# Performance work log

Measured on AMD Instinct MI355X. Metric: run time of the kernel, lower is better.

The kernel has to match this reference:

```python
import jax, jax.numpy as jnp
import numpy as np

B_, G_, H_ = 16, 4096, 128
D_INNER, D_STATE, NHEADS, HEADDIM, CHUNK, D_CONV = 256, 16, 4, 64, 64, 4
LATENT = 64
D_IN_PROJ = 2 * D_INNER + 2 * D_STATE + NHEADS  # 548
CONV_DIM = D_INNER + 2 * D_STATE                # 288
NLAYERS = 4  # [fwd0, fwd1, bwd0, bwd1]
EPS = 1e-5


def _segsum(x):
    # x: (..., T) -> (..., T, T) stable segment sums, -inf above diagonal
    T = x.shape[-1]
    xe = jnp.broadcast_to(x[..., None], x.shape + (T,))
    lo = jnp.tril(jnp.ones((T, T), bool), -1)
    s = jnp.cumsum(jnp.where(lo, xe, 0.0), axis=-2)
    keep = jnp.tril(jnp.ones((T, T), bool), 0)
    return jnp.where(keep, s, -jnp.inf)


def _ssd(x, A, B, C):
    # x: (b, L, h, p), A: (b, L, h), B/C: (b, L, n)  (single shared head for B/C)
    b, L, h, p = x.shape
    c = L // CHUNK
    x = x.reshape(b, c, CHUNK, h, p)
    A = A.reshape(b, c, CHUNK, h).transpose(0, 3, 1, 2)  # b h c l
    B = B.reshape(b, c, CHUNK, -1)                       # b c l n
    C = C.reshape(b, c, CHUNK, -1)
    A_cs = jnp.cumsum(A, axis=-1)
    Lmat = jnp.exp(_segsum(A))                           # b h c l s
    Y_diag = jnp.einsum('bcln,bcsn,bhcls,bcshp->bclhp', C, B, Lmat, x)
    decay_states = jnp.exp(A_cs[:, :, :, -1:] - A_cs)
    states = jnp.einsum('bcln,bhcl,bclhp->bchpn', B, decay_states, x)
    states = jnp.concatenate([jnp.zeros_like(states[:, :1]), states], axis=1)
    decay_chunk = jnp.exp(_segsum(jnp.pad(A_cs[:, :, :, -1], ((0, 0), (0, 0), (1, 0)))))
    new_states = jnp.einsum('bhzc,bchpn->bzhpn', decay_chunk, states)
    states = new_states[:, :-1]
    sdo = jnp.exp(A_cs)
    Y_off = jnp.einsum('bcln,bchpn,bhcl->bclhp', C, states, sdo)
    return (Y_diag + Y_off).reshape(b, L, h, p)


def _mamba2(u, Wi, cw, cb, dtb, Alog, Dp, nw, Wo):
    b, L, _ = u.shape
    zxbcdt = u @ Wi.T                                   # (b, L, 548)
    z = zxbcdt[..., :D_INNER]
    xBC = zxbcdt[..., D_INNER:D_INNER + CONV_DIM]
    dt = jax.nn.softplus(zxbcdt[..., D_INNER + CONV_DIM:] + dtb)  # (b, L, h)
    # depthwise causal conv1d, padding=d_conv-1, keep first L outputs
    xt = xBC.transpose(0, 2, 1)
    y = jax.lax.conv_general_dilated(xt, cw[:, None, :], (1,), [(D_CONV - 1, D_CONV - 1)],
                                     dimension_numbers=('NCH', 'OIH', 'NCH'),
                                     feature_group_count=CONV_DIM)
    xBC = jax.nn.silu((y[:, :, :L] + cb[None, :, None]).transpose(0, 2, 1))
    x = xBC[..., :D_INNER].reshape(b, L, NHEADS, HEADDIM)
    Bm = xBC[..., D_INNER:D_INNER + D_STATE]
    Cm = xBC[..., D_INNER + D_STATE:]
    A = -jnp.exp(Alog)                                  # (h,)
    yssd = _ssd(x * dt[..., None], A * dt, Bm, Cm)
    yssd = yssd + x * Dp[:, None]
    yf = yssd.reshape(b, L, D_INNER)
    yf = yf * jax.nn.silu(z)                            # gated RMSNorm
    yf = yf * jax.lax.rsqrt(jnp.mean(yf * yf, -1, keepdims=True) + EPS) * nw
    return yf @ Wo.T


def _forward(expression, noise, expr_w, expr_b, in_proj_w, conv_w, conv_b, dt_bias,
             A_log, D_par, norm_w, out_proj_w, fusion_w, fusion_b, lm_w, lm_b,
             lv_w, lv_b, gate_w, gate_b, outp_w, outp_b, reg_gate):
    x = expression[..., None] * expr_w[:, 0] + expr_b   # Linear(1, H) -> (b, G, H)
    fwd = x
    for i in (0, 1):
        fwd = _mamba2(fwd, in_proj_w[i], conv_w[i], conv_b[i], dt_bias[i],
                      A_log[i], D_par[i], norm_w[i], out_proj_w[i])
    bwd = x[:, ::-1]
    for i in (2, 3):
        bwd = _mamba2(bwd, in_proj_w[i], conv_w[i], conv_b[i], dt_bias[i],
                      A_log[i], D_par[i], norm_w[i], out_proj_w[i])
    bwd = bwd[:, ::-1]
    fused = jax.nn.gelu(jnp.concatenate([fwd, bwd], -1) @ fusion_w.T + fusion_b,
                        approximate=False)
    lm = fused @ lm_w.T + lm_b
    lv = fused @ lv_w.T + lv_b
    sample = lm + noise * jnp.exp(0.5 * lv)             # reparameterize
    gate = jax.nn.sigmoid(sample @ gate_w.T + gate_b)
    h = fused * gate
    pred = (h @ outp_w.T + outp_b)[..., 0] * jax.nn.sigmoid(reg_gate)
    return pred, lm, lv, sample


def setup_inputs() -> dict:
    key = jax.random.key(0)
    ks = jax.random.split(key, 24)
    def w(k, shape, s=0.02):
        return jax.random.normal(k, shape, jnp.float32) * s
    return dict(
        expression=jax.random.uniform(ks[0], (B_, G_), jnp.float32),
        noise=jax.random.normal(ks[1], (B_, G_, LATENT), jnp.float32),
        expr_w=w(ks[2], (H_, 1), 0.2), expr_b=w(ks[3], (H_,)),
        in_proj_w=w(ks[4], (NLAYERS, D_IN_PROJ, H_)),
        conv_w=w(ks[5], (NLAYERS, CONV_DIM, D_CONV), 0.1),
        conv_b=w(ks[6], (NLAYERS, CONV_DIM)),
        dt_bias=jax.random.uniform(ks[7], (NLAYERS, NHEADS), jnp.float32, -4.0, 1.0),
        A_log=jnp.full((NLAYERS, NHEADS), -jnp.log(2.0), jnp.float32),
        D_par=jnp.ones((NLAYERS, NHEADS), jnp.float32),
        norm_w=jnp.ones((NLAYERS, D_INNER), jnp.float32),
        out_proj_w=w(ks[8], (NLAYERS, H_, D_INNER)),
        fusion_w=w(ks[9], (H_, 2 * H_)), fusion_b=w(ks[10], (H_,)),
        lm_w=w(ks[11], (LATENT, H_)), lm_b=w(ks[12], (LATENT,)),
        lv_w=w(ks[13], (LATENT, H_)), lv_b=w(ks[14], (LATENT,)),
        gate_w=w(ks[15], (H_, LATENT)), gate_b=w(ks[16], (H_,)),
        outp_w=w(ks[17], (1, H_)), outp_b=w(ks[18], (1,)),
        reg_gate=w(ks[19], (G_,), 0.01),
    )


def reference(expression, noise, expr_w, expr_b, in_proj_w, conv_w, conv_b, dt_bias,
              A_log, D_par, norm_w, out_proj_w, fusion_w, fusion_b, lm_w, lm_b,
              lv_w, lv_b, gate_w, gate_b, outp_w, outp_b, reg_gate):
    return _forward(expression, noise, expr_w, expr_b, in_proj_w, conv_w, conv_b,
                    dt_bias, A_log, D_par, norm_w, out_proj_w, fusion_w, fusion_b,
                    lm_w, lm_b, lv_w, lv_b, gate_w, gate_b, outp_w, outp_b, reg_gate)
```

## Files before the change

kernel.cpp:

```cpp
#include <hip/hip_runtime.h>
#include <math.h>

#define HMOD 128
#define DIN 256
#define NHEADS 4
#define HD 64
#define DSTATE 16
#define NCH 64
#define CONVD 288
#define DPROJ 548
#define LAT 64
#define LSEQ 4096

typedef __attribute__((ext_vector_type(8))) short bf16x8;
typedef __attribute__((ext_vector_type(4))) float f32x4;
typedef __attribute__((ext_vector_type(8))) unsigned short u16x8;

__device__ __forceinline__ float sigm(float x){ return 1.0f/(1.0f+__expf(-x)); }
__device__ __forceinline__ float siluf(float x){ return x/(1.0f+__expf(-x)); }
__device__ __forceinline__ float softplusf(float x){ return (x>20.0f)? x : log1pf(expf(x)); }
__device__ __forceinline__ float geluf(float x){ return 0.5f*x*(1.0f+erff(x*0.70710678118654752440f)); }
__device__ __forceinline__ unsigned short f2bf(float x){
  unsigned int u = __float_as_uint(x);
  return (unsigned short)((u + 0x7FFFu + ((u>>16)&1u)) >> 16);
}
__device__ __forceinline__ float bf2f(unsigned short h){
  return __uint_as_float(((unsigned int)h)<<16);
}

__global__ __launch_bounds__(256) void cvt_kernel(const float* __restrict__ in,
  unsigned short* __restrict__ out, int n)
{
  int i = blockIdx.x*256 + threadIdx.x;
  if (i < n) out[i] = f2bf(in[i]);
}
__global__ __launch_bounds__(256) void cvt_nw_kernel(const float* __restrict__ in,
  const float* __restrict__ nw, unsigned short* __restrict__ out, int n)
{
  int i = blockIdx.x*256 + threadIdx.x;
  if (i < n){
    int k = i & 255;
    int li = i >> 15;
    out[i] = f2bf(in[i]*nw[li*256 + k]);
  }
}
__global__ __launch_bounds__(256) void cvt_cw_kernel(const float* __restrict__ in,
  float* __restrict__ out)
{
  int i = blockIdx.x*256 + threadIdx.x;
  if (i < 4608){
    int li = i/1152, r = i - li*1152;
    int ch = r>>2, k = r&3;
    out[li*1152 + k*CONVD + ch] = in[i];
  }
}

__global__ __launch_bounds__(256) void embed_kernel(const float* __restrict__ expr,
    const float* __restrict__ ew, const float* __restrict__ eb,
    unsigned short* __restrict__ actA, unsigned short* __restrict__ actB)
{
  int gid = blockIdx.x*256 + threadIdx.x;
  int m = gid >> 7, hh = gid & 127;
  int bl = m >> 12, g = m & 4095;
  unsigned short v = f2bf(expr[m]*ew[hh] + eb[hh]);
  actA[gid] = v;
  actB[(size_t)(((bl<<12) | (4095-g))<<7) + hh] = v;
}

template<int KDIM, int NT, int EPI>
__global__ __launch_bounds__(256) void gemm3(
    const unsigned short* __restrict__ A,
    const unsigned short* __restrict__ A2,
    const unsigned short* __restrict__ Wb,
    const float* __restrict__ bias,
    const float* __restrict__ bias2,
    const float* __restrict__ ssqp,
    unsigned short* __restrict__ ob1,
    unsigned short* __restrict__ ob2,
    float* __restrict__ of1,
    float* __restrict__ of2,
    const float* __restrict__ nzp,
    float* __restrict__ of3,
    int N, int ldc)
{
  __shared__ unsigned short Ws[64*(KDIM+8)];
  __shared__ unsigned short Cb[(EPI==5) ? 8 : 128*72];
  const int tid = threadIdx.x;
  const int m0 = blockIdx.x<<7;
  const int wid = tid>>6, lane = tid&63;
  const int la = lane&15, kq = lane>>4;
  const int mw = m0 + wid*32;

  bf16x8 af[KDIM/32][2];
  #pragma unroll
  for (int ki=0; ki<KDIM/32; ki++){
    int k = ki*32 + kq*8;
    #pragma unroll
    for (int mf=0; mf<2; mf++){
      int row = mw + mf*16 + la;
      const unsigned short* src;
      if (EPI==2){
        if (k < 128) src = A + (size_t)row*128 + k;
        else { int bl2=row>>12, t=row&4095; src = A2 + (size_t)(((bl2<<12)|(4095-t)))*128 + (k-128); }
      } else {
        src = A + (size_t)row*KDIM + k;
      }
      af[ki][mf] = *(const bf16x8*)src;
    }
  }
  float scv[2][4];
  if (EPI==4){
    #pragma unroll
    for (int mf=0; mf<2; mf++)
      #pragma unroll
      for (int r=0; r<4; r++){
        int m = mw + mf*16 + kq*4 + r;
        float s = ssqp[m*4]+ssqp[m*4+1]+ssqp[m*4+2]+ssqp[m*4+3];
        scv[mf][r] = rsqrtf(s*(1.0f/256.0f) + 1e-5f);
      }
  }
  float vlm[2][4][4];

  const int KD8 = KDIM/8;
  for (int nt=0; nt<NT; nt++){
    int n0 = (blockIdx.y*NT + nt)<<6;
    for (int ci = tid; ci < 64*KD8; ci += 256){
      int row = ci/KD8, kc = (ci - row*KD8)*8;
      int n = n0 + row;
      bf16x8 v = {0,0,0,0,0,0,0,0};
      if (n < N) v = *(const bf16x8*)&Wb[(size_t)n*KDIM + kc];
      *(bf16x8*)&Ws[row*(KDIM+8) + kc] = v;
    }
    __syncthreads();
    f32x4 acc[2][4] = {};
    #pragma unroll
    for (int ki=0; ki<KDIM/32; ki++){
      #pragma unroll
      for (int nf=0; nf<4; nf++){
        bf16x8 bfr = *(const bf16x8*)&Ws[(nf*16 + la)*(KDIM+8) + ki*32 + kq*8];
        #pragma unroll
        for (int mf=0; mf<2; mf++)
          acc[mf][nf] = __builtin_amdgcn_mfma_f32_16x16x32_bf16(af[ki][mf], bfr, acc[mf][nf], 0,0,0);
      }
    }
    #pragma unroll
    for (int mf=0; mf<2; mf++){
      #pragma unroll
      for (int nf=0; nf<4; nf++){
        #pragma unroll
        for (int r=0; r<4; r++){
          int m = mw + mf*16 + kq*4 + r;
          int row = wid*32 + mf*16 + kq*4 + r;
          int n = n0 + nf*16 + la;
          int col = nf*16 + la;
          float v = acc[mf][nf][r];
          if (EPI==1){
            if (n >= DIN+CONVD && n < DPROJ)
              of1[(size_t)m*NHEADS + (n-DIN-CONVD)] = softplusf(v + bias[n-DIN-CONVD]);
            else
              Cb[row*72 + col] = f2bf(v);
          } else if (EPI==2){
            Cb[row*72 + col] = f2bf(geluf(v + bias[n]));
          } else if (EPI==4){
            Cb[row*72 + col] = f2bf(v*scv[mf][r]);
          } else if (EPI==5){
            if (nt == 0){
              float lm = v + bias[col];
              vlm[mf][nf][r] = lm;
              of1[(size_t)m*64 + col] = lm;
            } else {
              float lv = v + bias2[col];
              of2[(size_t)m*64 + col] = lv;
              float nzv = nzp[(size_t)m*64 + col];
              of3[(size_t)m*64 + col] = fmaf(nzv, expf(0.5f*lv), vlm[mf][nf][r]);
            }
          }
        }
      }
    }
    if (EPI!=5){
      __syncthreads();
      #pragma unroll
      for (int j=0; j<4; j++){
        int row = (tid>>3) + j*32;
        int col0 = (tid&7)*8;
        int m = m0 + row;
        int nch = n0 + col0;
        u16x8 val = *(const u16x8*)&Cb[row*72 + col0];
        if (EPI==1){
          if (nch < DIN)            *(u16x8*)&ob1[(size_t)m*DIN + nch] = val;
          else if (nch < DIN+CONVD) *(u16x8*)&ob2[(size_t)m*CONVD + (nch-DIN)] = val;
        } else {
          *(u16x8*)&ob1[(size_t)m*ldc + nch] = val;
        }
      }
    }
    __syncthreads();
  }
}

__global__ __launch_bounds__(256) void conv_kernel(const unsigned short* __restrict__ xraw,
  const float* __restrict__ cwT, const float* __restrict__ cb,
  unsigned short* __restrict__ xconv)
{
  int gid = blockIdx.x*256 + threadIdx.x;
  int m = gid / 36, v = gid - (gid/36)*36;
  int ch0 = v*8;
  int t = m & 4095;
  float acc[8];
  float4 b0 = *(const float4*)&cb[ch0];
  float4 b1 = *(const float4*)&cb[ch0+4];
  acc[0]=b0.x; acc[1]=b0.y; acc[2]=b0.z; acc[3]=b0.w;
  acc[4]=b1.x; acc[5]=b1.y; acc[6]=b1.z; acc[7]=b1.w;
  #pragma unroll
  for (int k=0;k<4;k++){
    int tt = t - 3 + k;
    if (tt >= 0){
      u16x8 xv = *(const u16x8*)&xraw[(size_t)(m-3+k)*CONVD + ch0];
      float4 w0 = *(const float4*)&cwT[k*CONVD + ch0];
      float4 w1 = *(const float4*)&cwT[k*CONVD + ch0 + 4];
      float w[8] = {w0.x,w0.y,w0.z,w0.w,w1.x,w1.y,w1.z,w1.w};
      #pragma unroll
      for (int j=0;j<8;j++) acc[j] = fmaf(w[j], bf2f(xv[j]), acc[j]);
    }
  }
  u16x8 o;
  #pragma unroll
  for (int j=0;j<8;j++) o[j] = f2bf(siluf(acc[j]));
  *(u16x8*)&xconv[(size_t)m*CONVD + ch0] = o;
}

__global__ __launch_bounds__(256) void ssd_front(
  const unsigned short* __restrict__ xconv, const float* __restrict__ dtsp,
  const float* __restrict__ Alog,
  float* __restrict__ states_g, float* __restrict__ acs_g, float* __restrict__ atot_g)
{
  __shared__ __align__(16) unsigned short Xt[64*88];
  __shared__ __align__(16) unsigned short Raw[64*72];
  __shared__ __align__(16) unsigned short Braw[64*24];
  __shared__ __align__(16) unsigned short Bwt[16*88];
  __shared__ float acs_s[64], dts_s[64];
  const int bx = blockIdx.x;
  const int h = bx & 3, c = (bx>>2)&63, bl = bx>>8;
  const int tid = threadIdx.x;
  const int tokbase = (bl<<12) + (c<<6);

  if (tid < 64) {
    float dt = dtsp[(size_t)(tokbase+tid)*NHEADS + h];
    dts_s[tid] = dt;
    float xsc = -__expf(Alog[h]) * dt;
    #pragma unroll
    for (int off=1; off<64; off<<=1){ float v = __shfl_up(xsc, off); if (tid >= off) xsc += v; }
    acs_s[tid] = xsc;
    acs_g[(size_t)bx*64 + tid] = xsc;
  }
  #pragma unroll
  for (int i=0;i<2;i++){
    int idx = tid + (i<<8);
    int l = idx>>3, g = idx&7;
    *(u16x8*)&Raw[l*72 + g*8] = *(const u16x8*)&xconv[(size_t)(tokbase+l)*CONVD + h*64 + g*8];
  }
  if (tid < 128){
    int l = tid>>1, half = tid&1;
    *(u16x8*)&Braw[l*24 + half*8] = *(const u16x8*)&xconv[(size_t)(tokbase+l)*CONVD + 256 + half*8];
  }
  __syncthreads();
  const float atotv = acs_s[63];
  if (tid==0) atot_g[bx] = atotv;
  #pragma unroll
  for (int i=0;i<2;i++){
    int u = tid + (i<<8);
    int ch = u & 63, l0 = (u>>6)*8;
    u16x8 o;
    #pragma unroll
    for (int j=0;j<8;j++) o[j] = Raw[(l0+j)*72 + ch];
    *(u16x8*)&Xt[ch*88 + l0] = o;
  }
  if (tid < 128){
    int ch = tid & 15, l0 = (tid>>4)*8;
    u16x8 o;
    #pragma unroll
    for (int j=0;j<8;j++){
      int l = l0+j;
      o[j] = f2bf(bf2f(Braw[l*24 + ch]) * __expf(atotv - acs_s[l]) * dts_s[l]);
    }
    *(u16x8*)&Bwt[ch*88 + l0] = o;
  }
  __syncthreads();
  const int wid = tid>>6, lane = tid&63;
  const int la = lane&15, kq = lane>>4;
  f32x4 acc = {0.f,0.f,0.f,0.f};
  #pragma unroll
  for (int kt=0; kt<2; kt++){
    bf16x8 a = *(const bf16x8*)&Xt[(wid*16+la)*88 + kt*32+kq*8];
    bf16x8 b = *(const bf16x8*)&Bwt[la*88 + kt*32+kq*8];
    acc = __builtin_amdgcn_mfma_f32_16x16x32_bf16(a, b, acc, 0,0,0);
  }
  size_t base = (size_t)bx<<10;
  #pragma unroll
  for (int r=0;r<4;r++){
    int p = wid*16 + kq*4 + r;
    states_g[base + (size_t)p*16 + la] = acc[r];
  }
}

__global__ __launch_bounds__(256) void scan_kernel(float* __restrict__ states,
  const float* __restrict__ atot)
{
  int gid = blockIdx.x*256 + threadIdx.x;
  int inner = gid & 1023;
  int h = (gid>>10)&3;
  int bl = gid>>12;
  size_t base = (size_t)bl*262144 + h*1024 + inner;
  int abase = bl*256 + h;
  float v[64];
  #pragma unroll
  for (int c2=0;c2<64;c2++) v[c2] = states[base + (size_t)c2*4096];
  float S = 0.0f;
  #pragma unroll
  for (int c2=0;c2<64;c2++){
    states[base + (size_t)c2*4096] = S;
    S = __expf(atot[abase + c2*4])*S + v[c2];
  }
}

__global__ __launch_bounds__(256) void ssd_back(
  const unsigned short* __restrict__ xconv, const unsigned short* __restrict__ zb,
  const float* __restrict__ dtsp, const float* __restrict__ acs_g,
  const float* __restrict__ states, const float* __restrict__ Dp,
  unsigned short* __restrict__ yf, float* __restrict__ ssqp)
{
  __shared__ __align__(16) unsigned short U[2*64*72];
  __shared__ __align__(16) unsigned short CBS[3*64*40];
  __shared__ float acs_s[64], dts_s[64];
  unsigned short* Xt = U;
  unsigned short* Sb = U + 64*72;
  unsigned short* Cp = CBS;
  unsigned short* Bp = CBS + 64*40;
  unsigned short* Sp = CBS + 2*64*40;
  float* Yl = (float*)U;
  const int bx = blockIdx.x;
  const int h = bx & 3, c = (bx>>2)&63, bl = bx>>8;
  const int tid = threadIdx.x;
  const int tokbase = (bl<<12) + (c<<6);

  if (tid < 64) {
    dts_s[tid] = dtsp[(size_t)(tokbase+tid)*NHEADS + h];
    acs_s[tid] = acs_g[(size_t)bx*64 + tid];
  }
  for (int i = tid; i < 1024; i += 256){
    int l = i>>4, k = 16 + (i&15);
    Cp[l*40+k] = 0; Bp[l*40+k] = 0; Sp[l*40+k] = 0;
  }
  #pragma unroll
  for (int i=0;i<2;i++){
    int idx = tid + (i<<8);
    int l = idx>>3, g = idx&7;
    *(u16x8*)&Sb[l*72 + g*8] = *(const u16x8*)&xconv[(size_t)(tokbase+l)*CONVD + h*64 + g*8];
  }
  {
    int l = tid>>2, part = tid&3;
    u16x8 vv = *(const u16x8*)&xconv[(size_t)(tokbase+l)*CONVD + 256 + part*8];
    if (part < 2) *(u16x8*)&Bp[l*40 + part*8] = vv;
    else          *(u16x8*)&Cp[l*40 + (part-2)*8] = vv;
  }
  #pragma unroll
  for (int i=0;i<4;i++){
    int e = tid + (i<<8);
    int p = e>>4, n = e&15;
    Sp[p*40+n] = f2bf(states[((size_t)bx<<10) + e]);
  }
  __syncthreads();
  #pragma unroll
  for (int i=0;i<2;i++){
    int u = tid + (i<<8);
    int ch = u & 63, l0 = (u>>6)*8;
    u16x8 o;
    #pragma unroll
    for (int j=0;j<8;j++) o[j] = Sb[(l0+j)*72 + ch];
    *(u16x8*)&Xt[ch*72 + l0] = o;
  }
  __syncthreads();

  const int wid = tid>>6, lane = tid&63;
  const int la = lane&15, kq = lane>>4;
  const int L0 = wid*16;
  const f32x4 zero4 = {0.f,0.f,0.f,0.f};
  const float Dh = Dp[h];

  {
    bf16x8 a = *(const bf16x8*)&Cp[(L0+la)*40 + kq*8];
    f32x4 cbacc[4];
    #pragma unroll
    for (int nf=0; nf<4; nf++){
      bf16x8 b = *(const bf16x8*)&Bp[(nf*16+la)*40 + kq*8];
      cbacc[nf] = __builtin_amdgcn_mfma_f32_16x16x32_bf16(a, b, zero4, 0,0,0);
    }
    #pragma unroll
    for (int nf=0; nf<4; nf++){
      #pragma unroll
      for (int r=0; r<4; r++){
        int l = L0 + kq*4 + r, s = nf*16 + la;
        float v = 0.f;
        if (s <= l) v = __expf(acs_s[l]-acs_s[s])*dts_s[s]*cbacc[nf][r];
        if (s == l) v += Dh;
        Sb[l*72 + s] = f2bf(v);
      }
    }
  }
  f32x4 ya[4];
  {
    bf16x8 a = *(const bf16x8*)&Cp[(L0+la)*40 + kq*8];
    #pragma unroll
    for (int nf=0; nf<4; nf++){
      bf16x8 b = *(const bf16x8*)&Sp[(nf*16+la)*40 + kq*8];
      ya[nf] = __builtin_amdgcn_mfma_f32_16x16x32_bf16(a, b, zero4, 0,0,0);
    }
    float eal[4];
    #pragma unroll
    for (int r=0; r<4; r++) eal[r] = __expf(acs_s[L0 + kq*4 + r]);
    #pragma unroll
    for (int nf=0; nf<4; nf++)
      #pragma unroll
      for (int r=0; r<4; r++) ya[nf][r] *= eal[r];
  }
  #pragma unroll
  for (int kt=0; kt<2; kt++){
    bf16x8 a = *(const bf16x8*)&Sb[(L0+la)*72 + kt*32+kq*8];
    #pragma unroll
    for (int nf=0; nf<4; nf++){
      bf16x8 b = *(const bf16x8*)&Xt[(nf*16+la)*72 + kt*32+kq*8];
      ya[nf] = __builtin_amdgcn_mfma_f32_16x16x32_bf16(a, b, ya[nf], 0,0,0);
    }
  }
  __syncthreads();
  #pragma unroll
  for (int nf=0; nf<4; nf++){
    #pragma unroll
    for (int r=0; r<4; r++){
      int l = L0 + kq*4 + r, p = nf*16 + la;
      Yl[l*68 + p] = ya[nf][r];
    }
  }
  __syncthreads();
  #pragma unroll
  for (int i=0;i<2;i++){
    int u = tid + (i<<8);
    int l = u>>3, g = u&7;
    size_t gidx = (size_t)(tokbase+l)*DIN + (h<<6) + g*8;
    u16x8 z8 = *(const u16x8*)&zb[gidx];
    u16x8 o8;
    float ps = 0.f;
    #pragma unroll
    for (int j=0;j<8;j++){
      float y = Yl[l*68 + g*8 + j];
      float zv = bf2f(z8[j]);
      float yv = y * zv * sigm(zv);
      o8[j] = f2bf(yv);
      ps = fmaf(yv, yv, ps);
    }
    *(u16x8*)&yf[gidx] = o8;
    ps += __shfl_xor(ps, 1); ps += __shfl_xor(ps, 2); ps += __shfl_xor(ps, 4);
    if (g == 0) ssqp[(size_t)(tokbase+l)*NHEADS + h] = ps;
  }
}

__global__ __launch_bounds__(256) void predgate_kernel(
  const unsigned short* __restrict__ fused, const float* __restrict__ sample,
  const unsigned short* __restrict__ gwb, const float* __restrict__ gb,
  const float* __restrict__ ow, const float* __restrict__ ob,
  const float* __restrict__ rg, float* __restrict__ pred)
{
  __shared__ __align__(16) unsigned short Ws[64*72];
  __shared__ __align__(16) float Gp[128*68];
  const int tid = threadIdx.x;
  const int m0 = blockIdx.x<<7;
  const int wid = tid>>6, lane = tid&63;
  const int la = lane&15, kq = lane>>4;
  const int mw = m0 + wid*32;

  bf16x8 af[2][2];
  #pragma unroll
  for (int ki=0; ki<2; ki++){
    int k = ki*32 + kq*8;
    #pragma unroll
    for (int mf=0; mf<2; mf++){
      int row = mw + mf*16 + la;
      float4 s0 = *(const float4*)&sample[(size_t)row*64 + k];
      float4 s1 = *(const float4*)&sample[(size_t)row*64 + k + 4];
      bf16x8 o;
      o[0]=(short)f2bf(s0.x); o[1]=(short)f2bf(s0.y); o[2]=(short)f2bf(s0.z); o[3]=(short)f2bf(s0.w);
      o[4]=(short)f2bf(s1.x); o[5]=(short)f2bf(s1.y); o[6]=(short)f2bf(s1.z); o[7]=(short)f2bf(s1.w);
      af[ki][mf] = o;
    }
  }
  const float ob0 = ob[0];
  const int prow = tid>>1, phalf = tid&1;
  float rs = 0.f;

  #pragma unroll
  for (int nt=0; nt<2; nt++){
    int n0 = nt<<6;
    #pragma unroll
    for (int i=0;i<2;i++){
      int slot = tid + (i<<8);
      int row = slot>>3, g = slot&7;
      *(u16x8*)&Ws[row*72 + g*8] = *(const u16x8*)&gwb[(size_t)(n0+row)*64 + g*8];
    }
    __syncthreads();
    f32x4 acc[2][4] = {};
    #pragma unroll
    for (int ki=0; ki<2; ki++){
      #pragma unroll
      for (int nf=0; nf<4; nf++){
        bf16x8 bfr = *(const bf16x8*)&Ws[(nf*16 + la)*72 + ki*32 + kq*8];
        #pragma unroll
        for (int mf=0; mf<2; mf++)
          acc[mf][nf] = __builtin_amdgcn_mfma_f32_16x16x32_bf16(af[ki][mf], bfr, acc[mf][nf], 0,0,0);
      }
    }
    #pragma unroll
    for (int mf=0; mf<2; mf++){
      #pragma unroll
      for (int nf=0; nf<4; nf++){
        #pragma unroll
        for (int r=0; r<4; r++){
          int row = wid*32 + mf*16 + kq*4 + r;
          int col = nf*16 + la;
          int n = n0 + col;
          Gp[row*68 + col] = sigm(acc[mf][nf][r] + gb[n]) * ow[n];
        }
      }
    }
    __syncthreads();
    #pragma unroll
    for (int q=0; q<4; q++){
      int col0 = phalf*32 + q*8;
      u16x8 f8 = *(const u16x8*)&fused[(size_t)(m0+prow)*128 + n0 + col0];
      float4 g0 = *(const float4*)&Gp[prow*68 + col0];
      float4 g1 = *(const float4*)&Gp[prow*68 + col0 + 4];
      rs = fmaf(bf2f(f8[0]), g0.x, rs); rs = fmaf(bf2f(f8[1]), g0.y, rs);
      rs = fmaf(bf2f(f8[2]), g0.z, rs); rs = fmaf(bf2f(f8[3]), g0.w, rs);
      rs = fmaf(bf2f(f8[4]), g1.x, rs); rs = fmaf(bf2f(f8[5]), g1.y, rs);
      rs = fmaf(bf2f(f8[6]), g1.z, rs); rs = fmaf(bf2f(f8[7]), g1.w, rs);
    }
    __syncthreads();
  }
  rs += __shfl_xor(rs, 1);
  if (phalf == 0){
    int m = m0 + prow;
    pred[m] = (rs + ob0) * sigm(rg[m & 4095]);
  }
}

extern "C" void kernel_launch(void* const* d_in, const int* in_sizes, int n_in,
                              void* d_out, int out_size, void* d_ws, size_t ws_size,
                              hipStream_t stream)
{
  const float* expr      = (const float*)d_in[0];
  const float* noise     = (const float*)d_in[1];
  const float* expr_w    = (const float*)d_in[2];
  const float* expr_b    = (const float*)d_in[3];
  const float* in_proj_w = (const float*)d_in[4];
  const float* conv_w    = (const float*)d_in[5];
  const float* conv_b    = (const float*)d_in[6];
  const float* dt_bias   = (const float*)d_in[7];
  const float* A_log     = (const float*)d_in[8];
  const float* D_par     = (const float*)d_in[9];
  const float* norm_w    = (const float*)d_in[10];
  const float* out_proj_w= (const float*)d_in[11];
  const float* fusion_w  = (const float*)d_in[12];
  const float* fusion_b  = (const float*)d_in[13];
  const float* lm_w      = (const float*)d_in[14];
  const float* lm_b      = (const float*)d_in[15];
  const float* lv_w      = (const float*)d_in[16];
  const float* lv_b      = (const float*)d_in[17];
  const float* gate_w    = (const float*)d_in[18];
  const float* gate_b    = (const float*)d_in[19];
  const float* outp_w    = (const float*)d_in[20];
  const float* outp_b    = (const float*)d_in[21];
  const float* reg_gate  = (const float*)d_in[22];

  const size_t WBYTES = 956416;
  int BG = 0;
  const int cands[5] = {16, 8, 4, 2, 1};
  for (int ci = 0; ci < 5; ci++) {
    int c2 = cands[ci];
    size_t MGc = (size_t)c2 * LSEQ;
    size_t need = WBYTES + MGc*2992 + (size_t)c2*1024 + 256;
    if (need <= ws_size) { BG = c2; break; }
  }
  if (!BG) return;
  const size_t MG = (size_t)BG * LSEQ;

  unsigned short* wip = (unsigned short*)d_ws;
  unsigned short* wop = wip + 280576;
  unsigned short* wfu = wop + 131072;
  unsigned short* wlm = wfu + 32768;
  unsigned short* wlv = wlm + 8192;
  unsigned short* wgw = wlv + 8192;
  float* cwT   = (float*)(wgw + 8192);
  float* dtsp  = (float*)((char*)d_ws + WBYTES);
  float* acs   = dtsp + MG*4;
  float* atot  = acs  + MG*4;
  float* states= atot + (size_t)BG*256;
  float* ssqp  = states + MG*64;
  unsigned short* zb    = (unsigned short*)(ssqp + MG*4);
  unsigned short* xrawb = zb    + MG*256;
  unsigned short* xcv   = xrawb + MG*288;
  unsigned short* actA  = xcv   + MG*288;
  unsigned short* actB  = actA  + MG*128;
  unsigned short* yfb   = actB  + MG*128;
  unsigned short* fusedbf = yfb;

  float* out_pred_g = (float*)d_out;
  float* out_lm_g   = out_pred_g + (size_t)16*LSEQ;
  float* out_lv_g   = out_lm_g   + (size_t)16*LSEQ*LAT;
  float* out_samp_g = out_lv_g   + (size_t)16*LSEQ*LAT;

  cvt_kernel<<<(280576+255)/256, 256, 0, stream>>>(in_proj_w, wip, 280576);
  cvt_nw_kernel<<<131072/256,    256, 0, stream>>>(out_proj_w, norm_w, wop, 131072);
  cvt_kernel<<<32768/256,        256, 0, stream>>>(fusion_w, wfu, 32768);
  cvt_kernel<<<8192/256,         256, 0, stream>>>(lm_w, wlm, 8192);
  cvt_kernel<<<8192/256,         256, 0, stream>>>(lv_w, wlv, 8192);
  cvt_kernel<<<8192/256,         256, 0, stream>>>(gate_w, wgw, 8192);
  cvt_cw_kernel<<<(4608+255)/256, 256, 0, stream>>>(conv_w, cwT);

  for (int b0 = 0; b0 < 16; b0 += BG) {
    float* out_pred = out_pred_g + (size_t)b0*LSEQ;
    float* out_lm   = out_lm_g   + (size_t)b0*LSEQ*LAT;
    float* out_lv   = out_lv_g   + (size_t)b0*LSEQ*LAT;
    float* out_samp = out_samp_g + (size_t)b0*LSEQ*LAT;
    const float* nz = noise      + (size_t)b0*LSEQ*LAT;

    embed_kernel<<<(MG*128)/256, 256, 0, stream>>>(expr + (size_t)b0*LSEQ, expr_w, expr_b, actA, actB);

    for (int li = 0; li < 4; li++) {
      unsigned short* u = (li < 2) ? actA : actB;
      const unsigned short* Wi = wip + (size_t)li*DPROJ*HMOD;
      const unsigned short* Wo = wop + (size_t)li*HMOD*DIN;
      const float* cwTl = cwT + (size_t)li*1152;
      const float* cb   = conv_b + (size_t)li*CONVD;
      const float* dtb  = dt_bias + (size_t)li*NHEADS;
      const float* Al   = A_log + (size_t)li*NHEADS;
      const float* Dl   = D_par + (size_t)li*NHEADS;

      gemm3<128,1,1><<<dim3(MG/128, 9), 256, 0, stream>>>(u, nullptr, Wi, dtb, nullptr, nullptr, zb, xrawb, dtsp, nullptr, nullptr, nullptr, DPROJ, 0);
      conv_kernel<<<(MG*36)/256, 256, 0, stream>>>(xrawb, cwTl, cb, xcv);
      ssd_front<<<BG*256, 256, 0, stream>>>(xcv, dtsp, Al, states, acs, atot);
      scan_kernel<<<(BG*LSEQ)/256, 256, 0, stream>>>(states, atot);
      ssd_back<<<BG*256, 256, 0, stream>>>(xcv, zb, dtsp, acs, states, Dl, yfb, ssqp);
      gemm3<256,1,4><<<dim3(MG/128, 2), 256, 0, stream>>>(yfb, nullptr, Wo, nullptr, nullptr, ssqp, u, nullptr, nullptr, nullptr, nullptr, nullptr, HMOD, HMOD);
    }

    gemm3<256,1,2><<<dim3(MG/128, 2), 256, 0, stream>>>(actA, actB, wfu, fusion_b, nullptr, nullptr, fusedbf, nullptr, nullptr, nullptr, nullptr, nullptr, HMOD, HMOD);
    gemm3<128,2,5><<<dim3(MG/128, 1), 256, 0, stream>>>(fusedbf, nullptr, wlm, lm_b, lv_b, nullptr, nullptr, nullptr, out_lm, out_lv, nz, out_samp, 128, LAT);
    predgate_kernel<<<MG/128, 256, 0, stream>>>(fusedbf, out_samp, wgw, gate_b, outp_w, outp_b, reg_gate, out_pred);
  }
}
```

Baseline: 637.7 us.

## Swap MFMA operands for row-contiguous epilogue and vectorize GEMM stores

```diff
diff --git a/kernel.cpp b/kernel.cpp
--- a/kernel.cpp
+++ b/kernel.cpp
@@ -15,6 +15,7 @@
 typedef __attribute__((ext_vector_type(8))) short bf16x8;
 typedef __attribute__((ext_vector_type(4))) float f32x4;
 typedef __attribute__((ext_vector_type(8))) unsigned short u16x8;
+typedef __attribute__((ext_vector_type(4))) unsigned short u16x4;
 
 __device__ __forceinline__ float sigm(float x){ return 1.0f/(1.0f+__expf(-x)); }
 __device__ __forceinline__ float siluf(float x){ return x/(1.0f+__expf(-x)); }
@@ -84,7 +85,7 @@
     int N, int ldc)
 {
   __shared__ unsigned short Ws[64*(KDIM+8)];
-  __shared__ unsigned short Cb[(EPI==5) ? 8 : 128*72];
+  __shared__ __align__(16) unsigned short Cb[(EPI==5) ? 8 : 128*72];
   const int tid = threadIdx.x;
   const int m0 = blockIdx.x<<7;
   const int wid = tid>>6, lane = tid&63;
@@ -108,18 +109,16 @@
       af[ki][mf] = *(const bf16x8*)src;
     }
   }
-  float scv[2][4];
+  float scv[2];
   if (EPI==4){
     #pragma unroll
-    for (int mf=0; mf<2; mf++)
-      #pragma unroll
-      for (int r=0; r<4; r++){
-        int m = mw + mf*16 + kq*4 + r;
-        float s = ssqp[m*4]+ssqp[m*4+1]+ssqp[m*4+2]+ssqp[m*4+3];
-        scv[mf][r] = rsqrtf(s*(1.0f/256.0f) + 1e-5f);
-      }
-  }
-  float vlm[2][4][4];
+    for (int mf=0; mf<2; mf++){
+      int m = mw + mf*16 + la;
+      float4 s4 = *(const float4*)&ssqp[m*4];
+      scv[mf] = rsqrtf((s4.x+s4.y+s4.z+s4.w)*(1.0f/256.0f) + 1e-5f);
+    }
+  }
+  f32x4 vlm[2][4];
 
   const int KD8 = KDIM/8;
   for (int nt=0; nt<NT; nt++){
@@ -137,43 +136,59 @@
     for (int ki=0; ki<KDIM/32; ki++){
       #pragma unroll
       for (int nf=0; nf<4; nf++){
-        bf16x8 bfr = *(const bf16x8*)&Ws[(nf*16 + la)*(KDIM+8) + ki*32 + kq*8];
+        bf16x8 wfr = *(const bf16x8*)&Ws[(nf*16 + la)*(KDIM+8) + ki*32 + kq*8];
         #pragma unroll
         for (int mf=0; mf<2; mf++)
-          acc[mf][nf] = __builtin_amdgcn_mfma_f32_16x16x32_bf16(af[ki][mf], bfr, acc[mf][nf], 0,0,0);
+          acc[mf][nf] = __builtin_amdgcn_mfma_f32_16x16x32_bf16(wfr, af[ki][mf], acc[mf][nf], 0,0,0);
       }
     }
     #pragma unroll
     for (int mf=0; mf<2; mf++){
       #pragma unroll
       for (int nf=0; nf<4; nf++){
-        #pragma unroll
-        for (int r=0; r<4; r++){
-          int m = mw + mf*16 + kq*4 + r;
-          int row = wid*32 + mf*16 + kq*4 + r;
-          int n = n0 + nf*16 + la;
-          int col = nf*16 + la;
-          float v = acc[mf][nf][r];
-          if (EPI==1){
-            if (n >= DIN+CONVD && n < DPROJ)
-              of1[(size_t)m*NHEADS + (n-DIN-CONVD)] = softplusf(v + bias[n-DIN-CONVD]);
-            else
-              Cb[row*72 + col] = f2bf(v);
-          } else if (EPI==2){
-            Cb[row*72 + col] = f2bf(geluf(v + bias[n]));
-          } else if (EPI==4){
-            Cb[row*72 + col] = f2bf(v*scv[mf][r]);
-          } else if (EPI==5){
-            if (nt == 0){
-              float lm = v + bias[col];
-              vlm[mf][nf][r] = lm;
-              of1[(size_t)m*64 + col] = lm;
-            } else {
-              float lv = v + bias2[col];
-              of2[(size_t)m*64 + col] = lv;
-              float nzv = nzp[(size_t)m*64 + col];
-              of3[(size_t)m*64 + col] = fmaf(nzv, expf(0.5f*lv), vlm[mf][nf][r]);
+        int m   = mw + mf*16 + la;
+        int row = wid*32 + mf*16 + la;
+        int colb = nf*16 + kq*4;
+        int nb  = n0 + colb;
+        f32x4 v = acc[mf][nf];
+        if (EPI==1){
+          if (nb >= DIN+CONVD){
+            if (nb < DPROJ){
+              float4 o;
+              o.x = softplusf(v[0] + bias[0]); o.y = softplusf(v[1] + bias[1]);
+              o.z = softplusf(v[2] + bias[2]); o.w = softplusf(v[3] + bias[3]);
+              *(float4*)&of1[(size_t)m*NHEADS] = o;
             }
+          } else {
+            u16x4 p; p[0]=f2bf(v[0]); p[1]=f2bf(v[1]); p[2]=f2bf(v[2]); p[3]=f2bf(v[3]);
+            *(u16x4*)&Cb[row*72 + colb] = p;
+          }
+        } else if (EPI==2){
+          float4 b4 = *(const float4*)&bias[nb];
+          u16x4 p;
+          p[0]=f2bf(geluf(v[0]+b4.x)); p[1]=f2bf(geluf(v[1]+b4.y));
+          p[2]=f2bf(geluf(v[2]+b4.z)); p[3]=f2bf(geluf(v[3]+b4.w));
+          *(u16x4*)&Cb[row*72 + colb] = p;
+        } else if (EPI==4){
+          u16x4 p;
+          p[0]=f2bf(v[0]*scv[mf]); p[1]=f2bf(v[1]*scv[mf]);
+          p[2]=f2bf(v[2]*scv[mf]); p[3]=f2bf(v[3]*scv[mf]);
+          *(u16x4*)&Cb[row*72 + colb] = p;
+        } else if (EPI==5){
+          if (nt == 0){
+            float4 b4 = *(const float4*)&bias[colb];
+            f32x4 lm; lm[0]=v[0]+b4.x; lm[1]=v[1]+b4.y; lm[2]=v[2]+b4.z; lm[3]=v[3]+b4.w;
+            vlm[mf][nf] = lm;
+            *(f32x4*)&of1[(size_t)m*64 + colb] = lm;
+          } else {
+            float4 b4 = *(const float4*)&bias2[colb];
+            f32x4 lv; lv[0]=v[0]+b4.x; lv[1]=v[1]+b4.y; lv[2]=v[2]+b4.z; lv[3]=v[3]+b4.w;
+            *(f32x4*)&of2[(size_t)m*64 + colb] = lv;
+            f32x4 nz = *(const f32x4*)&nzp[(size_t)m*64 + colb];
+            f32x4 sp;
+            #pragma unroll
+            for (int j=0;j<4;j++) sp[j] = fmaf(nz[j], expf(0.5f*lv[j]), vlm[mf][nf][j]);
+            *(f32x4*)&of3[(size_t)m*64 + colb] = sp;
           }
         }
       }
@@ -645,7 +660,7 @@
       const float* Al   = A_log + (size_t)li*NHEADS;
       const float* Dl   = D_par + (size_t)li*NHEADS;
 
-      gemm3<128,1,1><<<dim3(MG/128, 9), 256, 0, stream>>>(u, nullptr, Wi, dtb, nullptr, nullptr, zb, xrawb, dtsp, nullptr, nullptr, nullptr, DPROJ, 0);
+      gemm3<128,3,1><<<dim3(MG/128, 3), 256, 0, stream>>>(u, nullptr, Wi, dtb, nullptr, nullptr, zb, xrawb, dtsp, nullptr, nullptr, nullptr, DPROJ, 0);
       conv_kernel<<<(MG*36)/256, 256, 0, stream>>>(xrawb, cwTl, cb, xcv);
       ssd_front<<<BG*256, 256, 0, stream>>>(xcv, dtsp, Al, states, acs, atot);
       scan_kernel<<<(BG*LSEQ)/256, 256, 0, stream>>>(states, atot);
```

Result: faster. 612.8 us (-3.9%).
